# Optimization experiments

Hardware: AMD Instinct MI355X
Metric: run time of the kernel (lower is better)

The kernel has to match this reference:

```python
import jax, jax.numpy as jnp
import numpy as np

B, S, D = 16, 2048, 128


def setup_inputs() -> dict:
    k = jax.random.key(0)
    k1, k2, k3, k4 = jax.random.split(k, 4)
    query = jax.random.normal(k1, (B, S, D), dtype=jnp.float32)
    key = jax.random.normal(k2, (B, S, D), dtype=jnp.float32)
    value = jax.random.normal(k3, (B, S, D), dtype=jnp.float32)
    # per-query tensor-valued inverse scale; shift away from zero for stable division
    inv_scale_factor = jax.random.uniform(k4, (B, S, 1), dtype=jnp.float32) + 0.5
    dropout_p = jnp.float32(0.1)
    return {"query": query, "key": key, "value": value,
            "inv_scale_factor": inv_scale_factor, "dropout_p": dropout_p}


def reference(query, key, value, inv_scale_factor, dropout_p):
    # QK^T: [B, Sq, Sk]
    qk = jnp.einsum('bqd,bkd->bqk', query, key)
    # tensor-valued scale divide (broadcast [B, Sq, 1] over keys)
    scaled_qk = qk / inv_scale_factor
    softmax_qk = jax.nn.softmax(scaled_qk, axis=-1)
    # dropout with a fixed RNG key (deterministic reference)
    keep_prob = 1.0 - dropout_p
    mask = jax.random.bernoulli(jax.random.key(42), keep_prob, softmax_qk.shape)
    dropout_qk = jnp.where(mask, softmax_qk / keep_prob, jnp.float32(0.0))
    # AV: [B, Sq, Dv]
    return jnp.einsum('bqk,bkv->bqv', dropout_qk, value)
```

## Files before the change

### kernel.cpp

```cpp
#include <hip/hip_runtime.h>
#include <stdint.h>


#define B_ 16
#define S_ 2048
#define D_ 128
#define TQ 128
#define TK 64
#define KSTR 136
#define VSTR 72
#define PSTR 40

typedef float f32x4 __attribute__((ext_vector_type(4)));
typedef _Float16 f16x8 __attribute__((ext_vector_type(8)));
typedef _Float16 f16x2 __attribute__((ext_vector_type(2)));

union F32R { float4 q[4]; float f[16]; };

#define DPP_ROR(x, ctrl) \
  __int_as_float(__builtin_amdgcn_update_dpp(0, __float_as_int(x), (ctrl), 0xf, 0xf, true))
__device__ __forceinline__ float row16_max(float x) {
  x = fmaxf(x, DPP_ROR(x, 0x128));
  x = fmaxf(x, DPP_ROR(x, 0x124));
  x = fmaxf(x, DPP_ROR(x, 0x122));
  x = fmaxf(x, DPP_ROR(x, 0x121));
  return x;
}
__device__ __forceinline__ float row16_sum(float x) {
  x += DPP_ROR(x, 0x128);
  x += DPP_ROR(x, 0x124);
  x += DPP_ROR(x, 0x122);
  x += DPP_ROR(x, 0x121);
  return x;
}

__device__ __forceinline__ uint2 threefry2x32_0_42(uint32_t x0, uint32_t x1) {
  const uint32_t k0 = 0u, k1 = 42u;
  const uint32_t k2 = 0x1BD11BDAu ^ k0 ^ k1;
  x0 += k0; x1 += k1;
#define TFR(r) { x0 += x1; x1 = __builtin_rotateleft32(x1, r); x1 ^= x0; }
  TFR(13) TFR(15) TFR(26) TFR(6)
  x0 += k1; x1 += k2 + 1u;
  TFR(17) TFR(29) TFR(16) TFR(24)
  x0 += k2; x1 += k0 + 2u;
  TFR(13) TFR(15) TFR(26) TFR(6)
  x0 += k0; x1 += k1 + 3u;
  TFR(17) TFR(29) TFR(16) TFR(24)
  x0 += k1; x1 += k2 + 4u;
  TFR(13) TFR(15) TFR(26) TFR(6)
  x0 += k2; x1 += k0 + 5u;
#undef TFR
  return make_uint2(x0, x1);
}

__device__ __forceinline__ uint32_t jax_bits(uint32_t j) {
  const uint2 tf = threefry2x32_0_42(0u, j);
  return tf.x ^ tf.y;
}

__global__ __launch_bounds__(512, 2)
void attn_mfma_kernel(const float* __restrict__ Q, const float* __restrict__ K,
                      const float* __restrict__ V, const float* __restrict__ ISF,
                      const float* __restrict__ DP, float* __restrict__ OUT) {
  extern __shared__ __align__(16) char smem[];
  _Float16* const sK  = (_Float16*)smem;
  _Float16* const sVT = (_Float16*)(smem + 17408);
  _Float16* const sP  = (_Float16*)(smem + 35840);
  float* const sO1 = (float*)smem;
  float* const sM1 = (float*)(smem + 65536);
  float* const sL1 = (float*)(smem + 66048);

  const int t    = threadIdx.x;
  const int lane = t & 63;
  const int l15  = lane & 15;
  const int quad = lane >> 4;
  const int w    = t >> 6;
  const int qg   = w & 3;
  const int kph  = w >> 2;
  const int b    = blockIdx.y;
  const int qb   = blockIdx.x * TQ + qg * 32;

  const float kp = 1.0f - DP[0];
  const uint32_t TH9 = (__float_as_uint(1.0f + kp) & 0x7FFFFFu) << 9;

  float m_[2][4], l_[2][4];
  uint32_t jq[2][4];
  #pragma unroll
  for (int sub = 0; sub < 2; ++sub)
    #pragma unroll
    for (int r = 0; r < 4; ++r) {
      m_[sub][r] = -INFINITY;
      l_[sub][r] = 0.0f;
      jq[sub][r] = ((uint32_t)b << 22)
                 + (uint32_t)(qb + sub * 16 + quad * 4 + r) * (uint32_t)S_;
    }

  f16x8 qf[2][4];
  #pragma unroll
  for (int sub = 0; sub < 2; ++sub) {
    const int qrow = qb + sub * 16 + l15;
    const float qs = 1.4426950408889634f / ISF[b * S_ + qrow];
    const float* qp = Q + ((size_t)(b * S_ + qrow)) * D_;
    #pragma unroll
    for (int c = 0; c < 4; ++c) {
      const float4 a  = *(const float4*)(qp + c * 32 + quad * 8);
      const float4 d2 = *(const float4*)(qp + c * 32 + quad * 8 + 4);
      const float xs[8] = {a.x, a.y, a.z, a.w, d2.x, d2.y, d2.z, d2.w};
      f16x8 h;
      #pragma unroll
      for (int j = 0; j < 8; ++j) h[j] = (_Float16)(xs[j] * qs);
      qf[sub][c] = h;
    }
  }

  f32x4 accO[2][8];
  #pragma unroll
  for (int sub = 0; sub < 2; ++sub)
    #pragma unroll
    for (int i = 0; i < 8; ++i) accO[sub][i] = (f32x4){0.f, 0.f, 0.f, 0.f};

  _Float16* const pwv = &sP[w * 32 * PSTR];

  const int krow = t >> 3, kcol = (t & 7) * 16;
  const int vp = t & 31, dseg = (t >> 5) * 8;

  F32R kreg;
  F32R vreg;

#define ISSUE_LOADS(KT)                                                        \
  {                                                                            \
    const float4* gk4 = (const float4*)(K +                                    \
        ((size_t)(b * S_ + (KT) * TK + krow)) * D_ + kcol);                    \
    _Pragma("unroll") for (int i = 0; i < 4; ++i) kreg.q[i] = gk4[i];          \
    const float4* gv4 = (const float4*)(V +                                    \
        ((size_t)(b * S_ + (KT) * TK + 2 * vp)) * D_ + dseg);                  \
    _Pragma("unroll") for (int i = 0; i < 2; ++i) {                            \
      vreg.q[i] = gv4[i];                                                      \
      vreg.q[i + 2] = gv4[i + 32];             \
    }                                                                          \
  }

  ISSUE_LOADS(0)

  for (int kt = 0; kt < S_ / TK; ++kt) {
    __syncthreads();

    {
      #pragma unroll
      for (int g = 0; g < 2; ++g) {
        f16x8 h;
        #pragma unroll
        for (int j = 0; j < 8; ++j) h[j] = (_Float16)kreg.f[g * 8 + j];
        *(f16x8*)&sK[krow * KSTR + kcol + g * 8] = h;
      }
    }
    {
      #pragma unroll
      for (int d = 0; d < 8; ++d) {
        f16x2 h = {(_Float16)vreg.f[d], (_Float16)vreg.f[8 + d]};
        *(f16x2*)&sVT[(dseg + d) * VSTR + 2 * vp] = h;
      }
    }
    __syncthreads();

    if (kt + 1 < S_ / TK) ISSUE_LOADS(kt + 1)

    f32x4 s[2][2];
    #pragma unroll
    for (int n = 0; n < 2; ++n) {
      f32x4 a0 = (f32x4){0.f, 0.f, 0.f, 0.f};
      f32x4 a1 = (f32x4){0.f, 0.f, 0.f, 0.f};
      #pragma unroll
      for (int c = 0; c < 4; ++c) {
        const f16x8 bh = *(const f16x8*)&sK[(kph * 32 + n * 16 + l15) * KSTR
                                            + c * 32 + quad * 8];
        a0 = __builtin_amdgcn_mfma_f32_16x16x32_f16(qf[0][c], bh, a0, 0, 0, 0);
        a1 = __builtin_amdgcn_mfma_f32_16x16x32_f16(qf[1][c], bh, a1, 0, 0, 0);
      }
      s[0][n] = a0;
      s[1][n] = a1;
    }

    float mx[2][4];
    int changed = 0;
    #pragma unroll
    for (int sub = 0; sub < 2; ++sub)
      #pragma unroll
      for (int r = 0; r < 4; ++r) {
        mx[sub][r] = row16_max(fmaxf(s[sub][0][r], s[sub][1][r]));
        changed |= (mx[sub][r] > m_[sub][r]);
      }
    if (__ballot(changed) != 0ull) {
      #pragma unroll
      for (int sub = 0; sub < 2; ++sub)
        #pragma unroll
        for (int r = 0; r < 4; ++r) {
          const float mnew = fmaxf(m_[sub][r], mx[sub][r]);
          const float alpha = __builtin_amdgcn_exp2f(m_[sub][r] - mnew);
          m_[sub][r] = mnew;
          l_[sub][r] *= alpha;
          #pragma unroll
          for (int i = 0; i < 8; ++i) accO[sub][i][r] *= alpha;
        }
    }
    #pragma unroll
    for (int sub = 0; sub < 2; ++sub)
      #pragma unroll
      for (int r = 0; r < 4; ++r) {
        const float p0 = __builtin_amdgcn_exp2f(s[sub][0][r] - m_[sub][r]);
        const float p1 = __builtin_amdgcn_exp2f(s[sub][1][r] - m_[sub][r]);
        s[sub][0][r] = p0;
        s[sub][1][r] = p1;
        l_[sub][r] += row16_sum(p0 + p1);
      }

    #pragma unroll
    for (int sub = 0; sub < 2; ++sub)
      #pragma unroll
      for (int n = 0; n < 2; ++n) {
        const int col = n * 16 + l15;
        const uint32_t jcol = (uint32_t)(kt * TK + kph * 32 + col);
        #pragma unroll
        for (int r = 0; r < 4; ++r) {
          const uint32_t bits = jax_bits(jq[sub][r] + jcol);
          const float pf = (bits < TH9) ? s[sub][n][r] : 0.0f;
          pwv[(sub * 16 + quad * 4 + r) * PSTR + col] = (_Float16)pf;
        }
      }
    __threadfence_block();

    {
      const f16x8 ap0 = *(const f16x8*)&pwv[l15 * PSTR + quad * 8];
      const f16x8 ap1 = *(const f16x8*)&pwv[(16 + l15) * PSTR + quad * 8];
      #pragma unroll
      for (int d8 = 0; d8 < 8; ++d8) {
        const f16x8 bv = *(const f16x8*)&sVT[(d8 * 16 + l15) * VSTR
                                             + kph * 32 + quad * 8];
        accO[0][d8] = __builtin_amdgcn_mfma_f32_16x16x32_f16(ap0, bv, accO[0][d8], 0, 0, 0);
        accO[1][d8] = __builtin_amdgcn_mfma_f32_16x16x32_f16(ap1, bv, accO[1][d8], 0, 0, 0);
      }
    }
  }
#undef ISSUE_LOADS

  __syncthreads();
  if (kph == 1) {
    #pragma unroll
    for (int sub = 0; sub < 2; ++sub) {
      if (l15 == 0) {
        #pragma unroll
        for (int r = 0; r < 4; ++r) {
          const int gr = qg * 32 + sub * 16 + quad * 4 + r;
          sM1[gr] = m_[sub][r];
          sL1[gr] = l_[sub][r];
        }
      }
      #pragma unroll
      for (int d8 = 0; d8 < 8; ++d8)
        #pragma unroll
        for (int r = 0; r < 4; ++r) {
          const int gr = qg * 32 + sub * 16 + quad * 4 + r;
          sO1[gr * D_ + d8 * 16 + l15] = accO[sub][d8][r];
        }
    }
  }
  __syncthreads();
  if (kph == 0) {
    #pragma unroll
    for (int sub = 0; sub < 2; ++sub) {
      float a0s[4], a1s[4];
      #pragma unroll
      for (int r = 0; r < 4; ++r) {
        const int gr = qg * 32 + sub * 16 + quad * 4 + r;
        const float m1  = sM1[gr];
        const float l1v = sL1[gr];
        const float mf = fmaxf(m_[sub][r], m1);
        const float a0 = __builtin_amdgcn_exp2f(m_[sub][r] - mf);
        const float a1 = __builtin_amdgcn_exp2f(m1 - mf);
        const float inv = 1.0f / ((a0 * l_[sub][r] + a1 * l1v) * kp);
        a0s[r] = a0 * inv;
        a1s[r] = a1 * inv;
      }
      #pragma unroll
      for (int d8 = 0; d8 < 8; ++d8)
        #pragma unroll
        for (int r = 0; r < 4; ++r) {
          const int gr = qg * 32 + sub * 16 + quad * 4 + r;
          const float o1 = sO1[gr * D_ + d8 * 16 + l15];
          OUT[((size_t)(b * S_ + blockIdx.x * TQ + gr)) * D_ + d8 * 16 + l15] =
              accO[sub][d8][r] * a0s[r] + o1 * a1s[r];
        }
    }
  }
}

extern "C" void kernel_launch(void* const* d_in, const int* in_sizes, int n_in,
                              void* d_out, int out_size, void* d_ws, size_t ws_size,
                              hipStream_t stream) {
  const float* q   = (const float*)d_in[0];
  const float* k   = (const float*)d_in[1];
  const float* v   = (const float*)d_in[2];
  const float* isf = (const float*)d_in[3];
  const float* dp  = (const float*)d_in[4];
  float* out = (float*)d_out;

  dim3 grid(S_ / TQ, B_);
  attn_mfma_kernel<<<grid, dim3(512), 66560, stream>>>(q, k, v, isf, dp, out);
}
```

Measured before the change: 288.1 us.

## Double-buffer K/V shared tiles and hoist dropout RNG before softmax

Splits the K and V^T shared-memory tiles into two buffers so the next tile is converted and stored while the current one is consumed, removing one barrier per iteration. The global prefetch now runs two tiles ahead. The threefry dropout bits are computed right after the QK MFMAs so the integer hash can overlap with MFMA latency. Shared memory grows from about 65 KB to 90 KB per block, which may cut blocks per CU below the launch-bounds target of 2, and the extra rb registers add register pressure.

```diff
diff --git a/kernel.cpp b/kernel.cpp
--- a/kernel.cpp
+++ b/kernel.cpp
@@ -7,6 +7,7 @@
 #define D_ 128
 #define TQ 128
 #define TK 64
+#define NT (S_ / TK)
 #define KSTR 136
 #define VSTR 72
 #define PSTR 40
@@ -63,9 +64,11 @@
                       const float* __restrict__ V, const float* __restrict__ ISF,
                       const float* __restrict__ DP, float* __restrict__ OUT) {
   extern __shared__ __align__(16) char smem[];
-  _Float16* const sK  = (_Float16*)smem;
-  _Float16* const sVT = (_Float16*)(smem + 17408);
-  _Float16* const sP  = (_Float16*)(smem + 35840);
+  _Float16* const sK0  = (_Float16*)smem;
+  _Float16* const sK1  = (_Float16*)(smem + 17408);
+  _Float16* const sVT0 = (_Float16*)(smem + 34816);
+  _Float16* const sVT1 = (_Float16*)(smem + 53248);
+  _Float16* const sP   = (_Float16*)(smem + 71680);
   float* const sO1 = (float*)smem;
   float* const sM1 = (float*)(smem + 65536);
   float* const sL1 = (float*)(smem + 66048);
@@ -140,30 +143,29 @@
     }                                                                          \
   }
 
+#define CONVERT_TO(KB, VB)                                                     \
+  {                                                                            \
+    _Pragma("unroll") for (int g = 0; g < 2; ++g) {                            \
+      f16x8 h;                                                                 \
+      _Pragma("unroll") for (int j = 0; j < 8; ++j)                            \
+        h[j] = (_Float16)kreg.f[g * 8 + j];                                    \
+      *(f16x8*)&(KB)[krow * KSTR + kcol + g * 8] = h;                          \
+    }                                                                          \
+    _Pragma("unroll") for (int d = 0; d < 8; ++d) {                            \
+      f16x2 h = {(_Float16)vreg.f[d], (_Float16)vreg.f[8 + d]};                \
+      *(f16x2*)&(VB)[(dseg + d) * VSTR + 2 * vp] = h;                          \
+    }                                                                          \
+  }
+
   ISSUE_LOADS(0)
-
-  for (int kt = 0; kt < S_ / TK; ++kt) {
-    __syncthreads();
-
-    {
-      #pragma unroll
-      for (int g = 0; g < 2; ++g) {
-        f16x8 h;
-        #pragma unroll
-        for (int j = 0; j < 8; ++j) h[j] = (_Float16)kreg.f[g * 8 + j];
-        *(f16x8*)&sK[krow * KSTR + kcol + g * 8] = h;
-      }
-    }
-    {
-      #pragma unroll
-      for (int d = 0; d < 8; ++d) {
-        f16x2 h = {(_Float16)vreg.f[d], (_Float16)vreg.f[8 + d]};
-        *(f16x2*)&sVT[(dseg + d) * VSTR + 2 * vp] = h;
-      }
-    }
-    __syncthreads();
-
-    if (kt + 1 < S_ / TK) ISSUE_LOADS(kt + 1)
+  CONVERT_TO(sK0, sVT0)
+  ISSUE_LOADS(1)
+  __syncthreads();
+
+  for (int kt = 0; kt < NT; ++kt) {
+    const int cur = kt & 1;
+    _Float16* const sKc = cur ? sK1 : sK0;
+    _Float16* const sVc = cur ? sVT1 : sVT0;
 
     f32x4 s[2][2];
     #pragma unroll
@@ -172,14 +174,25 @@
       f32x4 a1 = (f32x4){0.f, 0.f, 0.f, 0.f};
       #pragma unroll
       for (int c = 0; c < 4; ++c) {
-        const f16x8 bh = *(const f16x8*)&sK[(kph * 32 + n * 16 + l15) * KSTR
-                                            + c * 32 + quad * 8];
+        const f16x8 bh = *(const f16x8*)&sKc[(kph * 32 + n * 16 + l15) * KSTR
+                                             + c * 32 + quad * 8];
         a0 = __builtin_amdgcn_mfma_f32_16x16x32_f16(qf[0][c], bh, a0, 0, 0, 0);
         a1 = __builtin_amdgcn_mfma_f32_16x16x32_f16(qf[1][c], bh, a1, 0, 0, 0);
       }
       s[0][n] = a0;
       s[1][n] = a1;
     }
+
+    uint32_t rb[2][2][4];
+    #pragma unroll
+    for (int sub = 0; sub < 2; ++sub)
+      #pragma unroll
+      for (int n = 0; n < 2; ++n) {
+        const uint32_t jcol = (uint32_t)(kt * TK + kph * 32 + n * 16 + l15);
+        #pragma unroll
+        for (int r = 0; r < 4; ++r)
+          rb[sub][n][r] = jax_bits(jq[sub][r] + jcol);
+      }
 
     float mx[2][4];
     int changed = 0;
@@ -219,11 +232,9 @@
       #pragma unroll
       for (int n = 0; n < 2; ++n) {
         const int col = n * 16 + l15;
-        const uint32_t jcol = (uint32_t)(kt * TK + kph * 32 + col);
-        #pragma unroll
-        for (int r = 0; r < 4; ++r) {
-          const uint32_t bits = jax_bits(jq[sub][r] + jcol);
-          const float pf = (bits < TH9) ? s[sub][n][r] : 0.0f;
+        #pragma unroll
+        for (int r = 0; r < 4; ++r) {
+          const float pf = (rb[sub][n][r] < TH9) ? s[sub][n][r] : 0.0f;
           pwv[(sub * 16 + quad * 4 + r) * PSTR + col] = (_Float16)pf;
         }
       }
@@ -234,16 +245,24 @@
       const f16x8 ap1 = *(const f16x8*)&pwv[(16 + l15) * PSTR + quad * 8];
       #pragma unroll
       for (int d8 = 0; d8 < 8; ++d8) {
-        const f16x8 bv = *(const f16x8*)&sVT[(d8 * 16 + l15) * VSTR
+        const f16x8 bv = *(const f16x8*)&sVc[(d8 * 16 + l15) * VSTR
                                              + kph * 32 + quad * 8];
         accO[0][d8] = __builtin_amdgcn_mfma_f32_16x16x32_f16(ap0, bv, accO[0][d8], 0, 0, 0);
         accO[1][d8] = __builtin_amdgcn_mfma_f32_16x16x32_f16(ap1, bv, accO[1][d8], 0, 0, 0);
       }
     }
+
+    if (kt + 1 < NT) {
+      _Float16* const sKn = cur ? sK0 : sK1;
+      _Float16* const sVn = cur ? sVT0 : sVT1;
+      CONVERT_TO(sKn, sVn)
+      if (kt + 2 < NT) ISSUE_LOADS(kt + 2)
+    }
+    __syncthreads();
   }
 #undef ISSUE_LOADS
-
-  __syncthreads();
+#undef CONVERT_TO
+
   if (kph == 1) {
     #pragma unroll
     for (int sub = 0; sub < 2; ++sub) {
@@ -305,5 +324,5 @@
   float* out = (float*)d_out;
 
   dim3 grid(S_ / TQ, B_);
-  attn_mfma_kernel<<<grid, dim3(512), 66560, stream>>>(q, k, v, isf, dp, out);
-}
+  attn_mfma_kernel<<<grid, dim3(512), 92160, stream>>>(q, k, v, isf, dp, out);
+}
```

Result: faster. 276.7 us (-4.0%).
